# Optimization experiments

Hardware: AMD Instinct MI355X
Metric: run time of the kernel (lower is better)

Reference implementation:

```python
import jax, jax.numpy as jnp
import numpy as np

B, N, D = 4, 4096, 1024       # batch, seq_len, model dim
H, DH = 16, 64                # heads, dim per head
W = 256                       # sliding window size (causal: keys in [i-W+1, i])


def setup_inputs() -> dict:
    key = jax.random.key(0)
    k1, k2, k3 = jax.random.split(key, 3)
    x = jax.random.normal(k1, (B, N, D), dtype=jnp.float32)
    w_qkv = jax.random.normal(k2, (D, 3 * H * DH), dtype=jnp.float32) * (D ** -0.5)
    w_out = jax.random.normal(k3, (H * DH, D), dtype=jnp.float32) * ((H * DH) ** -0.5)
    return {"x": x, "w_qkv": w_qkv, "w_out": w_out}


def _sliding_window_attn(q, k, v):
    """Causal sliding-window attention, banded (block-local) computation.

    q,k,v: [BH, N, DH]; query i attends keys j with i-W+1 <= j <= i.
    Identical math to masking a full NxN score matrix with -finfo.max then softmax.
    """
    BH, n, dh = q.shape
    nb = n // W  # N is a multiple of W
    qb = q.reshape(BH, nb, W, dh)
    pad = jnp.zeros((BH, W, dh), q.dtype)
    kp = jnp.concatenate([pad, k], axis=1).reshape(BH, nb + 1, W, dh)
    vp = jnp.concatenate([pad, v], axis=1).reshape(BH, nb + 1, W, dh)
    # each query block sees previous block + current block of keys -> 2W keys
    kw = jnp.concatenate([kp[:, :-1], kp[:, 1:]], axis=2)  # [BH, nb, 2W, dh]
    vw = jnp.concatenate([vp[:, :-1], vp[:, 1:]], axis=2)
    scores = jnp.einsum('bnqd,bnkd->bnqk', qb, kw)  # [BH, nb, W, 2W]
    blk = jnp.arange(nb)[:, None, None]
    ii = jnp.arange(W)[None, :, None]
    jj = jnp.arange(2 * W)[None, None, :]
    # absolute key index = blk*W + jj - W ; absolute query index = blk*W + ii
    mask = (jj - W <= ii) & (jj >= ii + 1) & (blk * W + jj - W >= 0)
    neg = -jnp.finfo(scores.dtype).max  # matches torch max_neg_value
    scores = jnp.where(mask[None], scores, neg)
    attn = jax.nn.softmax(scores, axis=-1)
    out = jnp.einsum('bnqk,bnkd->bnqd', attn, vw)
    return out.reshape(BH, n, dh)


def reference(x, w_qkv, w_out):
    b, n, d = x.shape
    qkv = x @ w_qkv                      # [b, n, 3*H*DH]
    q, k, v = jnp.split(qkv, 3, axis=-1)

    def to_heads(t):  # b n (h d) -> (b h) n d
        return t.reshape(b, n, H, DH).transpose(0, 2, 1, 3).reshape(b * H, n, DH)

    q, k, v = map(to_heads, (q, k, v))
    q = q * (DH ** -0.5)                 # default scale = dim_head**-0.5
    out = _sliding_window_attn(q, k, v)  # [(b h), n, DH]
    out = out.reshape(b, H, n, DH).transpose(0, 2, 1, 3).reshape(b, n, H * DH)
    return out @ w_out
```

## Files before the change

kernel.cpp:

```cpp
#include <hip/hip_runtime.h>

typedef __attribute__((ext_vector_type(8))) short short8;
typedef __attribute__((ext_vector_type(4))) float floatx4;

#define AS1(p) ((const __attribute__((address_space(1))) void*)(uintptr_t)(p))
#define AS3(p) ((__attribute__((address_space(3))) void*)(unsigned int)(uintptr_t)(p))

__device__ __forceinline__ unsigned short f2bf(float f) {
    union { float f; unsigned int u; } v; v.f = f;
    unsigned int u = v.u;
    unsigned int r = (u + 0x7FFFu + ((u >> 16) & 1u)) >> 16;
    return (unsigned short)r;
}

__device__ __forceinline__ int pk_bf16(float a, float b) {
#if __has_builtin(__builtin_amdgcn_cvt_pk_bf16_f32)
    auto r = __builtin_amdgcn_cvt_pk_bf16_f32(a, b);
    int out; __builtin_memcpy(&out, &r, sizeof(int)); return out;
#else
    return (int)f2bf(a) | ((int)f2bf(b) << 16);
#endif
}

__global__ __launch_bounds__(256) void cvt_x(const float* __restrict__ src,
                                             unsigned short* __restrict__ dst, int n4) {
    int i = blockIdx.x * blockDim.x + threadIdx.x;
    if (i < n4) {
        float4 v = ((const float4*)src)[i];
        int2 o = {pk_bf16(v.x, v.y), pk_bf16(v.z, v.w)};
        ((int2*)dst)[i] = o;
    }
}

__global__ __launch_bounds__(256) void transpose_bf16(const float* __restrict__ src,
                                                      unsigned short* __restrict__ dst,
                                                      int R, int C) {
    __shared__ float tile[32][33];
    int c0 = blockIdx.x * 32, r0 = blockIdx.y * 32;
    int tc = threadIdx.x & 31, tr = (threadIdx.x >> 5) * 4;
#pragma unroll
    for (int i = 0; i < 4; ++i)
        tile[tr + i][tc] = src[(size_t)(r0 + tr + i) * C + c0 + tc];
    __syncthreads();
#pragma unroll
    for (int i = 0; i < 4; ++i)
        dst[(size_t)(c0 + tr + i) * R + r0 + tc] = f2bf(tile[tc][tr + i]);
}

template <bool OUT_BF16>
__global__ __launch_bounds__(512, 2) void gemm_bt256(const unsigned short* __restrict__ A,
                                                     const unsigned short* __restrict__ Bt,
                                                     void* __restrict__ Cout,
                                                     int M, int N, int K, int nbx) {
    __shared__ unsigned short Al[4][256 * 32];
    __shared__ unsigned short Bl[4][256 * 32];

    const int tid = threadIdx.x;
    const int wave = tid >> 6, lane = tid & 63, quad = lane >> 4, l15 = lane & 15;
    const int wm = wave >> 2, wn = wave & 3;

    const int nwg = (int)gridDim.x;
    const int q8 = nwg >> 3;
    const int wgid = (int)blockIdx.x;
    const int swz = (wgid & 7) * q8 + (wgid >> 3);
    const int bm = (swz / nbx) * 256;
    const int bn = (swz % nbx) * 256;

    floatx4 acc[8][4];
    const floatx4 z = {0.f, 0.f, 0.f, 0.f};
#pragma unroll
    for (int mi = 0; mi < 8; ++mi)
#pragma unroll
        for (int ni = 0; ni < 4; ++ni) acc[mi][ni] = z;

    const int d0 = tid, d1 = tid + 512;
    const int r0 = d0 >> 2, c0 = ((d0 & 3) ^ ((d0 >> 3) & 3)) * 8;
    const int r1 = d1 >> 2, c1 = ((d1 & 3) ^ ((d1 >> 3) & 3)) * 8;
    const unsigned short* As0 = A + (size_t)(bm + r0) * K + c0;
    const unsigned short* As1 = A + (size_t)(bm + r1) * K + c1;
    const unsigned short* Bs0 = Bt + (size_t)(bn + r0) * K + c0;
    const unsigned short* Bs1 = Bt + (size_t)(bn + r1) * K + c1;

    auto stageA = [&](int t) {
        const int s = t & 3, ko = t * 32;
        __builtin_amdgcn_global_load_lds(AS1(As0 + ko), AS3(&Al[s][d0 * 8]), 16, 0, 0);
        __builtin_amdgcn_global_load_lds(AS1(As1 + ko), AS3(&Al[s][d1 * 8]), 16, 0, 0);
    };
    auto stageB = [&](int t) {
        const int s = t & 3, ko = t * 32;
        __builtin_amdgcn_global_load_lds(AS1(Bs0 + ko), AS3(&Bl[s][d0 * 8]), 16, 0, 0);
        __builtin_amdgcn_global_load_lds(AS1(Bs1 + ko), AS3(&Bl[s][d1 * 8]), 16, 0, 0);
    };

    const int qc = (quad ^ ((l15 >> 1) & 3)) * 8;
    const int arow = wm * 128 + l15;
    const int brow = wn * 64 + l15;

    stageA(0); stageB(0);
    stageA(1); stageB(1);
    stageA(2); stageB(2);
    asm volatile("s_waitcnt vmcnt(8)" ::: "memory");
    __builtin_amdgcn_s_barrier();

    const int NT = K >> 5;
    for (int t = 0; t < NT; ++t) {
        const int s = t & 3;
        const unsigned short* Alp = Al[s];
        const unsigned short* Blp = Bl[s];
        short8 af[4], bf[4];

#pragma unroll
        for (int mi = 0; mi < 4; ++mi)
            af[mi] = *(const short8*)&Alp[(arow + mi * 16) * 32 + qc];
#pragma unroll
        for (int ni = 0; ni < 4; ++ni)
            bf[ni] = *(const short8*)&Blp[(brow + ni * 16) * 32 + qc];
        if (t + 3 < NT) stageA(t + 3);
        __builtin_amdgcn_s_barrier();
        __builtin_amdgcn_s_setprio(1);
#pragma unroll
        for (int mi = 0; mi < 4; ++mi)
#pragma unroll
            for (int ni = 0; ni < 4; ++ni)
                acc[mi][ni] = __builtin_amdgcn_mfma_f32_16x16x32_bf16(bf[ni], af[mi], acc[mi][ni], 0, 0, 0);
        __builtin_amdgcn_s_setprio(0);
        __builtin_amdgcn_s_barrier();

#pragma unroll
        for (int mi = 0; mi < 4; ++mi)
            af[mi] = *(const short8*)&Alp[(arow + 64 + mi * 16) * 32 + qc];
        if (t + 3 < NT) stageB(t + 3);
        __builtin_amdgcn_s_barrier();
        __builtin_amdgcn_s_setprio(1);
#pragma unroll
        for (int mi = 0; mi < 4; ++mi)
#pragma unroll
            for (int ni = 0; ni < 4; ++ni)
                acc[4 + mi][ni] = __builtin_amdgcn_mfma_f32_16x16x32_bf16(bf[ni], af[mi], acc[4 + mi][ni], 0, 0, 0);
        __builtin_amdgcn_s_setprio(0);

        if (t + 3 < NT)      asm volatile("s_waitcnt vmcnt(8)" ::: "memory");
        else if (t + 2 < NT) asm volatile("s_waitcnt vmcnt(4)" ::: "memory");
        else if (t + 1 < NT) asm volatile("s_waitcnt vmcnt(0)" ::: "memory");
        __builtin_amdgcn_s_barrier();
    }

#pragma unroll
    for (int mi = 0; mi < 8; ++mi) {
        const size_t row = (size_t)(bm + wm * 128 + mi * 16 + l15);
#pragma unroll
        for (int ni = 0; ni < 4; ++ni) {
            const size_t col = (size_t)(bn + wn * 64 + ni * 16 + quad * 4);
            if (OUT_BF16) {
                int2 val = {pk_bf16(acc[mi][ni][0], acc[mi][ni][1]),
                            pk_bf16(acc[mi][ni][2], acc[mi][ni][3])};
                *(int2*)((unsigned short*)Cout + row * N + col) = val;
            } else {
                *(float4*)((float*)Cout + row * N + col) = *(const float4*)&acc[mi][ni];
            }
        }
    }
}

__global__ __launch_bounds__(256, 3) void attn_swin(const unsigned short* __restrict__ qkv,
                                                    unsigned short* __restrict__ attn_out) {
    __shared__ unsigned short Klds[2][64 * 72];
    __shared__ unsigned short Vtl[2][64 * 72];

    const int blk = blockIdx.x, bh = blockIdx.y;
    const int b = bh >> 4, h = bh & 15;
    const int tid = threadIdx.x;
    const int wave = tid >> 6, lane = tid & 63, quad = lane >> 4, l15 = lane & 15;
    const int pair = wave >> 1;
    const int qoff = (wave & 1) * 32;
    const int qi_base = blk * 128 + wave * 32;
    const size_t seqbase = (size_t)b * 4096;

    short8 qf[2][2];
#pragma unroll
    for (int qt = 0; qt < 2; ++qt)
#pragma unroll
        for (int ks = 0; ks < 2; ++ks)
            qf[qt][ks] = *(const short8*)(qkv + (seqbase + qi_base + qt * 16 + l15) * 3072
                                          + h * 64 + ks * 32 + quad * 8);

    floatx4 o[2][4];
    const floatx4 z = {0.f, 0.f, 0.f, 0.f};
    float m_run[2], l_run[2];
#pragma unroll
    for (int qt = 0; qt < 2; ++qt) {
#pragma unroll
        for (int dt = 0; dt < 4; ++dt) o[qt][dt] = z;
        m_run[qt] = -1.0e30f; l_run[qt] = 0.f;
    }

    const int kwin0 = blk * 128 - 256;
    const int c0 = (blk >= 2) ? 0 : (4 - 2 * blk);
    const int cLo = pair, cHi = pair + 4;
    const int sk_key = tid >> 2, sk_g = (tid & 3) * 16;
    const int sv_key = tid & 63, sv_dg = (tid >> 6) * 16;
    const float SC = 0.18033688f;

    const int addrA = (((quad & 1) << 5) + l15) << 2;
    const int addrB = addrA + 64;
    const bool hiq = quad >= 2;

    int4 kvreg[4];
    auto load_kv = [&](int k0) {
        const int4* sk = (const int4*)(qkv + (seqbase + k0 + sk_key) * 3072 + 1024 + h * 64 + sk_g);
        kvreg[0] = sk[0]; kvreg[1] = sk[1];
        const int4* sv = (const int4*)(qkv + (seqbase + k0 + sv_key) * 3072 + 2048 + h * 64 + sv_dg);
        kvreg[2] = sv[0]; kvreg[3] = sv[1];
    };
    auto write_kv = [&](int buf) {
        *(int4*)&Klds[buf][sk_key * 72 + sk_g]     = kvreg[0];
        *(int4*)&Klds[buf][sk_key * 72 + sk_g + 8] = kvreg[1];
        union { unsigned short s[16]; int4 q[2]; } t;
        t.q[0] = kvreg[2]; t.q[1] = kvreg[3];
#pragma unroll
        for (int i = 0; i < 16; ++i) Vtl[buf][(sv_dg + i) * 72 + sv_key] = t.s[i];
    };

    load_kv(kwin0 + c0 * 64);
    write_kv(0);

    for (int c = c0; c < 6; ++c) {
        const int buf = (c - c0) & 1;
        __syncthreads();
        if (c < 5) load_kv(kwin0 + (c + 1) * 64);

        if (c >= cLo && c <= cHi) {
#pragma unroll
            for (int qt = 0; qt < 2; ++qt) {
                floatx4 sT[4];
#pragma unroll
                for (int ni = 0; ni < 4; ++ni) sT[ni] = z;
#pragma unroll
                for (int ks = 0; ks < 2; ++ks) {
#pragma unroll
                    for (int ni = 0; ni < 4; ++ni) {
                        short8 kf = *(const short8*)&Klds[buf][(ni * 16 + l15) * 72 + ks * 32 + quad * 8];
                        sT[ni] = __builtin_amdgcn_mfma_f32_16x16x32_bf16(kf, qf[qt][ks], sT[ni], 0, 0, 0);
                    }
                }

                short8 vf[4][2];
#pragma unroll
                for (int dt = 0; dt < 4; ++dt)
#pragma unroll
                    for (int ks = 0; ks < 2; ++ks)
                        vf[dt][ks] = *(const short8*)&Vtl[buf][(dt * 16 + l15) * 72 + ks * 32 + quad * 8];

                const int i64 = qoff + qt * 16 + l15;
                if (c == cLo) {
#pragma unroll
                    for (int ni = 0; ni < 4; ++ni) {
                        int jb = ni * 16 + quad * 4;
#pragma unroll
                        for (int r = 0; r < 4; ++r)
                            if (jb + r < i64 + 1) sT[ni][r] = -3.0e38f;
                    }
                } else if (c == cHi) {
#pragma unroll
                    for (int ni = 0; ni < 4; ++ni) {
                        int jb = ni * 16 + quad * 4;
#pragma unroll
                        for (int r = 0; r < 4; ++r)
                            if (jb + r > i64) sT[ni][r] = -3.0e38f;
                    }
                }

                float mx = -3.0e38f;
#pragma unroll
                for (int ni = 0; ni < 4; ++ni)
#pragma unroll
                    for (int r = 0; r < 4; ++r) mx = fmaxf(mx, sT[ni][r]);
                mx = fmaxf(mx, __shfl_xor(mx, 16));
                mx = fmaxf(mx, __shfl_xor(mx, 32));
                float mn = fmaxf(m_run[qt], mx * SC);
                float alpha = __builtin_amdgcn_exp2f(m_run[qt] - mn);
                m_run[qt] = mn;

                float ls = 0.f;
                int Pk[4][2];
#pragma unroll
                for (int ni = 0; ni < 4; ++ni) {
                    float p0 = __builtin_amdgcn_exp2f(fmaf(sT[ni][0], SC, -mn));
                    float p1 = __builtin_amdgcn_exp2f(fmaf(sT[ni][1], SC, -mn));
                    float p2 = __builtin_amdgcn_exp2f(fmaf(sT[ni][2], SC, -mn));
                    float p3 = __builtin_amdgcn_exp2f(fmaf(sT[ni][3], SC, -mn));
                    ls += (p0 + p1) + (p2 + p3);
                    Pk[ni][0] = pk_bf16(p0, p1);
                    Pk[ni][1] = pk_bf16(p2, p3);
                }
                ls += __shfl_xor(ls, 16);
                ls += __shfl_xor(ls, 32);
                l_run[qt] = l_run[qt] * alpha + ls;
#pragma unroll
                for (int dt = 0; dt < 4; ++dt)
#pragma unroll
                    for (int r = 0; r < 4; ++r) o[qt][dt][r] *= alpha;

#pragma unroll
                for (int ks = 0; ks < 2; ++ks) {
                    int a0 = __builtin_amdgcn_ds_bpermute(addrA, Pk[2 * ks][0]);
                    int b0 = __builtin_amdgcn_ds_bpermute(addrA, Pk[2 * ks + 1][0]);
                    int a1 = __builtin_amdgcn_ds_bpermute(addrA, Pk[2 * ks][1]);
                    int b1 = __builtin_amdgcn_ds_bpermute(addrA, Pk[2 * ks + 1][1]);
                    int a2 = __builtin_amdgcn_ds_bpermute(addrB, Pk[2 * ks][0]);
                    int b2 = __builtin_amdgcn_ds_bpermute(addrB, Pk[2 * ks + 1][0]);
                    int a3 = __builtin_amdgcn_ds_bpermute(addrB, Pk[2 * ks][1]);
                    int b3 = __builtin_amdgcn_ds_bpermute(addrB, Pk[2 * ks + 1][1]);
                    union { int i[4]; short8 v; } u;
                    u.i[0] = hiq ? b0 : a0;
                    u.i[1] = hiq ? b1 : a1;
                    u.i[2] = hiq ? b2 : a2;
                    u.i[3] = hiq ? b3 : a3;
#pragma unroll
                    for (int dt = 0; dt < 4; ++dt)
                        o[qt][dt] = __builtin_amdgcn_mfma_f32_16x16x32_bf16(vf[dt][ks], u.v, o[qt][dt], 0, 0, 0);
                }
            }
        }

        if (c < 5) write_kv(buf ^ 1);
    }

#pragma unroll
    for (int qt = 0; qt < 2; ++qt) {
        float rl = __builtin_amdgcn_rcpf(l_run[qt]);
        size_t rowb = (seqbase + qi_base + qt * 16 + l15) * 1024 + h * 64;
#pragma unroll
        for (int dt = 0; dt < 4; ++dt) {
            int2 val = {pk_bf16(o[qt][dt][0] * rl, o[qt][dt][1] * rl),
                        pk_bf16(o[qt][dt][2] * rl, o[qt][dt][3] * rl)};
            *(int2*)(attn_out + rowb + dt * 16 + quad * 4) = val;
        }
    }
}

extern "C" void kernel_launch(void* const* d_in, const int* in_sizes, int n_in,
                              void* d_out, int out_size, void* d_ws, size_t ws_size,
                              hipStream_t stream) {
    const float* x     = (const float*)d_in[0];
    const float* w_qkv = (const float*)d_in[1];
    const float* w_out = (const float*)d_in[2];
    float* out = (float*)d_out;

    unsigned short* xb    = (unsigned short*)d_ws;
    unsigned short* wqkvT = xb    + (size_t)16384 * 1024;
    unsigned short* woutT = wqkvT + (size_t)3072 * 1024;
    unsigned short* qkv   = woutT + (size_t)1024 * 1024;
    unsigned short* attn  = qkv   + (size_t)16384 * 3072;

    cvt_x<<<16384, 256, 0, stream>>>(x, xb, 4194304);
    transpose_bf16<<<dim3(96, 32), 256, 0, stream>>>(w_qkv, wqkvT, 1024, 3072);
    transpose_bf16<<<dim3(32, 32), 256, 0, stream>>>(w_out, woutT, 1024, 1024);
    gemm_bt256<true><<<768, 512, 0, stream>>>(xb, wqkvT, qkv, 16384, 3072, 1024, 12);
    attn_swin<<<dim3(32, 64), 256, 0, stream>>>(qkv, attn);
    gemm_bt256<false><<<256, 512, 0, stream>>>(attn, woutT, out, 16384, 1024, 1024, 4);
}
```

Measured before the change: 363.1 us.

## Software-pipeline LDS fragment loads across K iterations in bf16 GEMM

Restructures the GEMM main loop so LDS fragments for the next K-tile are loaded into double-buffered registers while the current tile's MFMAs run, cutting one barrier per iteration. The loop is manually unrolled by two to alternate register buffers, and the vmcnt waits are retuned to the new issue order. The cost is higher register pressure from the two fragment sets, and the unroll by two assumes NT is even.

```diff
diff --git a/kernel.cpp b/kernel.cpp
--- a/kernel.cpp
+++ b/kernel.cpp
@@ -81,6 +81,8 @@
     const unsigned short* Bs0 = Bt + (size_t)(bn + r0) * K + c0;
     const unsigned short* Bs1 = Bt + (size_t)(bn + r1) * K + c1;
 
+    const int NT = K >> 5;
+
     auto stageA = [&](int t) {
         const int s = t & 3, ko = t * 32;
         __builtin_amdgcn_global_load_lds(AS1(As0 + ko), AS3(&Al[s][d0 * 8]), 16, 0, 0);
@@ -102,47 +104,58 @@
     asm volatile("s_waitcnt vmcnt(8)" ::: "memory");
     __builtin_amdgcn_s_barrier();
 
-    const int NT = K >> 5;
-    for (int t = 0; t < NT; ++t) {
+    short8 afA[4], bfA[4], afB[4], bfB[4];
+#pragma unroll
+    for (int mi = 0; mi < 4; ++mi)
+        afA[mi] = *(const short8*)&Al[0][(arow + mi * 16) * 32 + qc];
+#pragma unroll
+    for (int ni = 0; ni < 4; ++ni)
+        bfA[ni] = *(const short8*)&Bl[0][(brow + ni * 16) * 32 + qc];
+
+    auto body = [&](int t, short8 (&caf)[4], short8 (&cbf)[4],
+                    short8 (&naf)[4], short8 (&nbf)[4]) {
         const int s = t & 3;
         const unsigned short* Alp = Al[s];
-        const unsigned short* Blp = Bl[s];
-        short8 af[4], bf[4];
-
+        if (t + 3 < NT) stageA(t + 3);
+        short8 af1[4];
 #pragma unroll
         for (int mi = 0; mi < 4; ++mi)
-            af[mi] = *(const short8*)&Alp[(arow + mi * 16) * 32 + qc];
-#pragma unroll
-        for (int ni = 0; ni < 4; ++ni)
-            bf[ni] = *(const short8*)&Blp[(brow + ni * 16) * 32 + qc];
-        if (t + 3 < NT) stageA(t + 3);
+            af1[mi] = *(const short8*)&Alp[(arow + 64 + mi * 16) * 32 + qc];
+        __builtin_amdgcn_s_setprio(1);
+#pragma unroll
+        for (int mi = 0; mi < 4; ++mi)
+#pragma unroll
+            for (int ni = 0; ni < 4; ++ni)
+                acc[mi][ni] = __builtin_amdgcn_mfma_f32_16x16x32_bf16(cbf[ni], caf[mi], acc[mi][ni], 0, 0, 0);
+        __builtin_amdgcn_s_setprio(0);
+        if (t + 3 < NT)       asm volatile("s_waitcnt vmcnt(6)" ::: "memory");
+        else if (t + 3 == NT) asm volatile("s_waitcnt vmcnt(4)" ::: "memory");
+        else                  asm volatile("s_waitcnt vmcnt(0)" ::: "memory");
         __builtin_amdgcn_s_barrier();
+        if (t + 1 < NT) {
+            const unsigned short* Aln = Al[(t + 1) & 3];
+            const unsigned short* Bln = Bl[(t + 1) & 3];
+#pragma unroll
+            for (int mi = 0; mi < 4; ++mi)
+                naf[mi] = *(const short8*)&Aln[(arow + mi * 16) * 32 + qc];
+#pragma unroll
+            for (int ni = 0; ni < 4; ++ni)
+                nbf[ni] = *(const short8*)&Bln[(brow + ni * 16) * 32 + qc];
+        }
+        if (t + 3 < NT) stageB(t + 3);
         __builtin_amdgcn_s_setprio(1);
 #pragma unroll
         for (int mi = 0; mi < 4; ++mi)
 #pragma unroll
             for (int ni = 0; ni < 4; ++ni)
-                acc[mi][ni] = __builtin_amdgcn_mfma_f32_16x16x32_bf16(bf[ni], af[mi], acc[mi][ni], 0, 0, 0);
+                acc[4 + mi][ni] = __builtin_amdgcn_mfma_f32_16x16x32_bf16(cbf[ni], af1[mi], acc[4 + mi][ni], 0, 0, 0);
         __builtin_amdgcn_s_setprio(0);
         __builtin_amdgcn_s_barrier();
-
-#pragma unroll
-        for (int mi = 0; mi < 4; ++mi)
-            af[mi] = *(const short8*)&Alp[(arow + 64 + mi * 16) * 32 + qc];
-        if (t + 3 < NT) stageB(t + 3);
-        __builtin_amdgcn_s_barrier();
-        __builtin_amdgcn_s_setprio(1);
-#pragma unroll
-        for (int mi = 0; mi < 4; ++mi)
-#pragma unroll
-            for (int ni = 0; ni < 4; ++ni)
-                acc[4 + mi][ni] = __builtin_amdgcn_mfma_f32_16x16x32_bf16(bf[ni], af[mi], acc[4 + mi][ni], 0, 0, 0);
-        __builtin_amdgcn_s_setprio(0);
-
-        if (t + 3 < NT)      asm volatile("s_waitcnt vmcnt(8)" ::: "memory");
-        else if (t + 2 < NT) asm volatile("s_waitcnt vmcnt(4)" ::: "memory");
-        else if (t + 1 < NT) asm volatile("s_waitcnt vmcnt(0)" ::: "memory");
-        __builtin_amdgcn_s_barrier();
+    };
+
+    for (int tt = 0; tt < NT; tt += 2) {
+        body(tt,     afA, bfA, afB, bfB);
+        body(tt + 1, afB, bfB, afA, bfA);
     }
 
 #pragma unroll
```

After: 362.4 us. No clear change (-0.2%).

## Restructure GEMM mainloop to K=64 tiles with half-tile double-buffered staging

Applied to the files above, without the earlier changes.

The GEMM mainloop now stages 64-wide K tiles into a 2-stage LDS buffer, split into 128-row halves, instead of 32-wide tiles in a 4-stage ring. Each K step runs four MFMA phases, and the A and B halves are prefetched at different distances (A one tile ahead, B two tiles ahead). The LDS swizzle is widened to an 8-way XOR to match. The aim is fewer loop iterations and barriers per unit of K work, with loads interleaved between MFMA phases. The cost is more register fragments live at once and tighter vmcnt and barrier ordering, where any mistake could cause races.

```diff
diff --git a/kernel.cpp b/kernel.cpp
--- a/kernel.cpp
+++ b/kernel.cpp
@@ -52,8 +52,8 @@
                                                      const unsigned short* __restrict__ Bt,
                                                      void* __restrict__ Cout,
                                                      int M, int N, int K, int nbx) {
-    __shared__ unsigned short Al[4][256 * 32];
-    __shared__ unsigned short Bl[4][256 * 32];
+    __shared__ unsigned short Ah[2][2][128 * 64];
+    __shared__ unsigned short Bh[2][2][128 * 64];
 
     const int tid = threadIdx.x;
     const int wave = tid >> 6, lane = tid & 63, quad = lane >> 4, l15 = lane & 15;
@@ -73,76 +73,110 @@
 #pragma unroll
         for (int ni = 0; ni < 4; ++ni) acc[mi][ni] = z;
 
-    const int d0 = tid, d1 = tid + 512;
-    const int r0 = d0 >> 2, c0 = ((d0 & 3) ^ ((d0 >> 3) & 3)) * 8;
-    const int r1 = d1 >> 2, c1 = ((d1 & 3) ^ ((d1 >> 3) & 3)) * 8;
-    const unsigned short* As0 = A + (size_t)(bm + r0) * K + c0;
-    const unsigned short* As1 = A + (size_t)(bm + r1) * K + c1;
-    const unsigned short* Bs0 = Bt + (size_t)(bn + r0) * K + c0;
-    const unsigned short* Bs1 = Bt + (size_t)(bn + r1) * K + c1;
-
-    auto stageA = [&](int t) {
-        const int s = t & 3, ko = t * 32;
-        __builtin_amdgcn_global_load_lds(AS1(As0 + ko), AS3(&Al[s][d0 * 8]), 16, 0, 0);
-        __builtin_amdgcn_global_load_lds(AS1(As1 + ko), AS3(&Al[s][d1 * 8]), 16, 0, 0);
+    const int r0 = tid >> 3;
+    const int cc = ((tid & 7) ^ ((tid >> 3) & 7)) * 8;
+    const unsigned short* Asrc = A + (size_t)(bm + r0) * K + cc;
+    const unsigned short* Bsrc = Bt + (size_t)(bn + r0) * K + cc;
+
+    const int NT = K >> 6;
+
+    auto stageA = [&](int t, int h) {
+        const unsigned short* s0 = Asrc + (size_t)h * 128 * K + t * 64;
+        unsigned short* d = &Ah[t & 1][h][tid * 8];
+        __builtin_amdgcn_global_load_lds(AS1(s0), AS3(d), 16, 0, 0);
+        __builtin_amdgcn_global_load_lds(AS1(s0 + (size_t)64 * K), AS3(d + 512 * 8), 16, 0, 0);
     };
-    auto stageB = [&](int t) {
-        const int s = t & 3, ko = t * 32;
-        __builtin_amdgcn_global_load_lds(AS1(Bs0 + ko), AS3(&Bl[s][d0 * 8]), 16, 0, 0);
-        __builtin_amdgcn_global_load_lds(AS1(Bs1 + ko), AS3(&Bl[s][d1 * 8]), 16, 0, 0);
+    auto stageB = [&](int t, int h) {
+        const unsigned short* s0 = Bsrc + (size_t)h * 128 * K + t * 64;
+        unsigned short* d = &Bh[t & 1][h][tid * 8];
+        __builtin_amdgcn_global_load_lds(AS1(s0), AS3(d), 16, 0, 0);
+        __builtin_amdgcn_global_load_lds(AS1(s0 + (size_t)64 * K), AS3(d + 512 * 8), 16, 0, 0);
     };
 
-    const int qc = (quad ^ ((l15 >> 1) & 3)) * 8;
-    const int arow = wm * 128 + l15;
-    const int brow = wn * 64 + l15;
-
-    stageA(0); stageB(0);
-    stageA(1); stageB(1);
-    stageA(2); stageB(2);
-    asm volatile("s_waitcnt vmcnt(8)" ::: "memory");
+    const int kc0 = ((quad     ) ^ (l15 & 7)) * 8;
+    const int kc1 = ((quad ^ 4) ^ (l15 & 7)) * 8;
+    const int brb = (wn & 1) * 64;
+
+    stageA(0, 0); stageA(0, 1);
+    stageB(0, 0); stageB(0, 1);
+    if (NT > 1) {
+        stageB(1, 0); stageB(1, 1);
+        asm volatile("s_waitcnt vmcnt(4)" ::: "memory");
+    } else {
+        asm volatile("s_waitcnt vmcnt(0)" ::: "memory");
+    }
     __builtin_amdgcn_s_barrier();
 
-    const int NT = K >> 5;
     for (int t = 0; t < NT; ++t) {
-        const int s = t & 3;
-        const unsigned short* Alp = Al[s];
-        const unsigned short* Blp = Bl[s];
-        short8 af[4], bf[4];
-
-#pragma unroll
-        for (int mi = 0; mi < 4; ++mi)
-            af[mi] = *(const short8*)&Alp[(arow + mi * 16) * 32 + qc];
+        const int s = t & 1;
+        const unsigned short* Ap = &Ah[s][wm][0];
+        const unsigned short* Bp = &Bh[s][wn >> 1][0];
+        short8 a0[4], a1[4], b0[4], b1[4];
+
+#pragma unroll
+        for (int mi = 0; mi < 4; ++mi)
+            a0[mi] = *(const short8*)&Ap[(mi * 16 + l15) * 64 + kc0];
 #pragma unroll
         for (int ni = 0; ni < 4; ++ni)
-            bf[ni] = *(const short8*)&Blp[(brow + ni * 16) * 32 + qc];
-        if (t + 3 < NT) stageA(t + 3);
+            b0[ni] = *(const short8*)&Bp[(brb + ni * 16 + l15) * 64 + kc0];
+        if (t + 1 < NT) stageA(t + 1, 0);
         __builtin_amdgcn_s_barrier();
         __builtin_amdgcn_s_setprio(1);
 #pragma unroll
         for (int mi = 0; mi < 4; ++mi)
 #pragma unroll
             for (int ni = 0; ni < 4; ++ni)
-                acc[mi][ni] = __builtin_amdgcn_mfma_f32_16x16x32_bf16(bf[ni], af[mi], acc[mi][ni], 0, 0, 0);
+                acc[mi][ni] = __builtin_amdgcn_mfma_f32_16x16x32_bf16(b0[ni], a0[mi], acc[mi][ni], 0, 0, 0);
         __builtin_amdgcn_s_setprio(0);
         __builtin_amdgcn_s_barrier();
 
 #pragma unroll
-        for (int mi = 0; mi < 4; ++mi)
-            af[mi] = *(const short8*)&Alp[(arow + 64 + mi * 16) * 32 + qc];
-        if (t + 3 < NT) stageB(t + 3);
+        for (int ni = 0; ni < 4; ++ni)
+            b1[ni] = *(const short8*)&Bp[(brb + ni * 16 + l15) * 64 + kc1];
+#pragma unroll
+        for (int mi = 0; mi < 4; ++mi)
+            a1[mi] = *(const short8*)&Ap[(64 + mi * 16 + l15) * 64 + kc0];
+        if (t + 1 < NT) stageA(t + 1, 1);
         __builtin_amdgcn_s_barrier();
         __builtin_amdgcn_s_setprio(1);
 #pragma unroll
         for (int mi = 0; mi < 4; ++mi)
 #pragma unroll
             for (int ni = 0; ni < 4; ++ni)
-                acc[4 + mi][ni] = __builtin_amdgcn_mfma_f32_16x16x32_bf16(bf[ni], af[mi], acc[4 + mi][ni], 0, 0, 0);
+                acc[4 + mi][ni] = __builtin_amdgcn_mfma_f32_16x16x32_bf16(b0[ni], a1[mi], acc[4 + mi][ni], 0, 0, 0);
         __builtin_amdgcn_s_setprio(0);
-
-        if (t + 3 < NT)      asm volatile("s_waitcnt vmcnt(8)" ::: "memory");
-        else if (t + 2 < NT) asm volatile("s_waitcnt vmcnt(4)" ::: "memory");
+        __builtin_amdgcn_s_barrier();
+
+#pragma unroll
+        for (int mi = 0; mi < 4; ++mi)
+            a0[mi] = *(const short8*)&Ap[(mi * 16 + l15) * 64 + kc1];
+        if (t + 2 < NT) stageB(t + 2, 0);
+        __builtin_amdgcn_s_barrier();
+        __builtin_amdgcn_s_setprio(1);
+#pragma unroll
+        for (int mi = 0; mi < 4; ++mi)
+#pragma unroll
+            for (int ni = 0; ni < 4; ++ni)
+                acc[mi][ni] = __builtin_amdgcn_mfma_f32_16x16x32_bf16(b1[ni], a0[mi], acc[mi][ni], 0, 0, 0);
+        __builtin_amdgcn_s_setprio(0);
+        __builtin_amdgcn_s_barrier();
+
+#pragma unroll
+        for (int mi = 0; mi < 4; ++mi)
+            a1[mi] = *(const short8*)&Ap[(64 + mi * 16 + l15) * 64 + kc1];
+        if (t + 2 < NT) stageB(t + 2, 1);
+        __builtin_amdgcn_s_barrier();
+        __builtin_amdgcn_s_setprio(1);
+#pragma unroll
+        for (int mi = 0; mi < 4; ++mi)
+#pragma unroll
+            for (int ni = 0; ni < 4; ++ni)
+                acc[4 + mi][ni] = __builtin_amdgcn_mfma_f32_16x16x32_bf16(b1[ni], a1[mi], acc[4 + mi][ni], 0, 0, 0);
+        __builtin_amdgcn_s_setprio(0);
+
+        if (t + 2 < NT)      asm volatile("s_waitcnt vmcnt(4)" ::: "memory");
         else if (t + 1 < NT) asm volatile("s_waitcnt vmcnt(0)" ::: "memory");
-        __builtin_amdgcn_s_barrier();
+        if (t + 1 < NT) __builtin_amdgcn_s_barrier();
     }
 
 #pragma unroll
```

Measured after the change: 361.0 us. Within noise of the previous version (-0.6%).

## Shrink GEMM tile to 128x256 with 4 waves and double-buffered LDS

Applied to the files above, without the earlier changes.

Replaces the 256x256, 8-wave, 4-stage GEMM with a 128x256 tile computed by 4 waves, each owning a 128x64 slice. LDS staging drops from four stages to two, with a single combined stage per k-step and a full vmcnt(0) wait before the barrier. The grids double so more workgroups can spread across CUs. In exchange, each tile reuses loaded data less, and the shallower prefetch can expose global-load latency.

```diff
diff --git a/kernel.cpp b/kernel.cpp
--- a/kernel.cpp
+++ b/kernel.cpp
@@ -48,22 +48,21 @@
 }
 
 template <bool OUT_BF16>
-__global__ __launch_bounds__(512, 2) void gemm_bt256(const unsigned short* __restrict__ A,
+__global__ __launch_bounds__(256, 2) void gemm_bt128(const unsigned short* __restrict__ A,
                                                      const unsigned short* __restrict__ Bt,
                                                      void* __restrict__ Cout,
                                                      int M, int N, int K, int nbx) {
-    __shared__ unsigned short Al[4][256 * 32];
-    __shared__ unsigned short Bl[4][256 * 32];
+    __shared__ unsigned short Asm[2][128 * 32];
+    __shared__ unsigned short Bsm[2][256 * 32];
 
     const int tid = threadIdx.x;
-    const int wave = tid >> 6, lane = tid & 63, quad = lane >> 4, l15 = lane & 15;
-    const int wm = wave >> 2, wn = wave & 3;
+    const int wn = tid >> 6, lane = tid & 63, quad = lane >> 4, l15 = lane & 15;
 
     const int nwg = (int)gridDim.x;
     const int q8 = nwg >> 3;
     const int wgid = (int)blockIdx.x;
     const int swz = (wgid & 7) * q8 + (wgid >> 3);
-    const int bm = (swz / nbx) * 256;
+    const int bm = (swz / nbx) * 128;
     const int bn = (swz % nbx) * 256;
 
     floatx4 acc[8][4];
@@ -73,81 +72,75 @@
 #pragma unroll
         for (int ni = 0; ni < 4; ++ni) acc[mi][ni] = z;
 
-    const int d0 = tid, d1 = tid + 512;
-    const int r0 = d0 >> 2, c0 = ((d0 & 3) ^ ((d0 >> 3) & 3)) * 8;
-    const int r1 = d1 >> 2, c1 = ((d1 & 3) ^ ((d1 >> 3) & 3)) * 8;
-    const unsigned short* As0 = A + (size_t)(bm + r0) * K + c0;
-    const unsigned short* As1 = A + (size_t)(bm + r1) * K + c1;
-    const unsigned short* Bs0 = Bt + (size_t)(bn + r0) * K + c0;
-    const unsigned short* Bs1 = Bt + (size_t)(bn + r1) * K + c1;
-
-    auto stageA = [&](int t) {
-        const int s = t & 3, ko = t * 32;
-        __builtin_amdgcn_global_load_lds(AS1(As0 + ko), AS3(&Al[s][d0 * 8]), 16, 0, 0);
-        __builtin_amdgcn_global_load_lds(AS1(As1 + ko), AS3(&Al[s][d1 * 8]), 16, 0, 0);
+    const int dA0 = tid, dA1 = tid + 256;
+    const int rA0 = dA0 >> 2, cA0 = ((dA0 & 3) ^ ((dA0 >> 3) & 3)) * 8;
+    const int rA1 = dA1 >> 2, cA1 = ((dA1 & 3) ^ ((dA1 >> 3) & 3)) * 8;
+    const unsigned short* Asrc0 = A + (size_t)(bm + rA0) * K + cA0;
+    const unsigned short* Asrc1 = A + (size_t)(bm + rA1) * K + cA1;
+    const unsigned short* Bsrc[4];
+    int dB[4];
+#pragma unroll
+    for (int j = 0; j < 4; ++j) {
+        dB[j] = tid + j * 256;
+        const int r = dB[j] >> 2, c = ((dB[j] & 3) ^ ((dB[j] >> 3) & 3)) * 8;
+        Bsrc[j] = Bt + (size_t)(bn + r) * K + c;
+    }
+
+    const int NT = K >> 5;
+
+    auto stage = [&](int t) {
+        const int s = t & 1, ko = t * 32;
+        __builtin_amdgcn_global_load_lds(AS1(Asrc0 + ko), AS3(&Asm[s][dA0 * 8]), 16, 0, 0);
+        __builtin_amdgcn_global_load_lds(AS1(Asrc1 + ko), AS3(&Asm[s][dA1 * 8]), 16, 0, 0);
+#pragma unroll
+        for (int j = 0; j < 4; ++j)
+            __builtin_amdgcn_global_load_lds(AS1(Bsrc[j] + ko), AS3(&Bsm[s][dB[j] * 8]), 16, 0, 0);
     };
-    auto stageB = [&](int t) {
-        const int s = t & 3, ko = t * 32;
-        __builtin_amdgcn_global_load_lds(AS1(Bs0 + ko), AS3(&Bl[s][d0 * 8]), 16, 0, 0);
-        __builtin_amdgcn_global_load_lds(AS1(Bs1 + ko), AS3(&Bl[s][d1 * 8]), 16, 0, 0);
-    };
 
     const int qc = (quad ^ ((l15 >> 1) & 3)) * 8;
-    const int arow = wm * 128 + l15;
     const int brow = wn * 64 + l15;
 
-    stageA(0); stageB(0);
-    stageA(1); stageB(1);
-    stageA(2); stageB(2);
-    asm volatile("s_waitcnt vmcnt(8)" ::: "memory");
+    stage(0);
+    asm volatile("s_waitcnt vmcnt(0)" ::: "memory");
     __builtin_amdgcn_s_barrier();
 
-    const int NT = K >> 5;
     for (int t = 0; t < NT; ++t) {
-        const int s = t & 3;
-        const unsigned short* Alp = Al[s];
-        const unsigned short* Blp = Bl[s];
-        short8 af[4], bf[4];
-
+        const int s = t & 1;
+        const unsigned short* Ap = Asm[s];
+        const unsigned short* Bp = Bsm[s];
+        if (t + 1 < NT) stage(t + 1);
+
+        short8 b[4], a0[4], a1[4];
+#pragma unroll
+        for (int ni = 0; ni < 4; ++ni)
+            b[ni] = *(const short8*)&Bp[(brow + ni * 16) * 32 + qc];
 #pragma unroll
         for (int mi = 0; mi < 4; ++mi)
-            af[mi] = *(const short8*)&Alp[(arow + mi * 16) * 32 + qc];
-#pragma unroll
-        for (int ni = 0; ni < 4; ++ni)
-            bf[ni] = *(const short8*)&Blp[(brow + ni * 16) * 32 + qc];
-        if (t + 3 < NT) stageA(t + 3);
+            a0[mi] = *(const short8*)&Ap[(mi * 16 + l15) * 32 + qc];
+#pragma unroll
+        for (int mi = 0; mi < 4; ++mi)
+            a1[mi] = *(const short8*)&Ap[(64 + mi * 16 + l15) * 32 + qc];
+
+        __builtin_amdgcn_s_setprio(1);
+#pragma unroll
+        for (int mi = 0; mi < 4; ++mi)
+#pragma unroll
+            for (int ni = 0; ni < 4; ++ni)
+                acc[mi][ni] = __builtin_amdgcn_mfma_f32_16x16x32_bf16(b[ni], a0[mi], acc[mi][ni], 0, 0, 0);
+#pragma unroll
+        for (int mi = 0; mi < 4; ++mi)
+#pragma unroll
+            for (int ni = 0; ni < 4; ++ni)
+                acc[4 + mi][ni] = __builtin_amdgcn_mfma_f32_16x16x32_bf16(b[ni], a1[mi], acc[4 + mi][ni], 0, 0, 0);
+        __builtin_amdgcn_s_setprio(0);
+
+        asm volatile("s_waitcnt vmcnt(0)" ::: "memory");
         __builtin_amdgcn_s_barrier();
-        __builtin_amdgcn_s_setprio(1);
-#pragma unroll
-        for (int mi = 0; mi < 4; ++mi)
-#pragma unroll
-            for (int ni = 0; ni < 4; ++ni)
-                acc[mi][ni] = __builtin_amdgcn_mfma_f32_16x16x32_bf16(bf[ni], af[mi], acc[mi][ni], 0, 0, 0);
-        __builtin_amdgcn_s_setprio(0);
-        __builtin_amdgcn_s_barrier();
-
-#pragma unroll
-        for (int mi = 0; mi < 4; ++mi)
-            af[mi] = *(const short8*)&Alp[(arow + 64 + mi * 16) * 32 + qc];
-        if (t + 3 < NT) stageB(t + 3);
-        __builtin_amdgcn_s_barrier();
-        __builtin_amdgcn_s_setprio(1);
-#pragma unroll
-        for (int mi = 0; mi < 4; ++mi)
-#pragma unroll
-            for (int ni = 0; ni < 4; ++ni)
-                acc[4 + mi][ni] = __builtin_amdgcn_mfma_f32_16x16x32_bf16(bf[ni], af[mi], acc[4 + mi][ni], 0, 0, 0);
-        __builtin_amdgcn_s_setprio(0);
-
-        if (t + 3 < NT)      asm volatile("s_waitcnt vmcnt(8)" ::: "memory");
-        else if (t + 2 < NT) asm volatile("s_waitcnt vmcnt(4)" ::: "memory");
-        else if (t + 1 < NT) asm volatile("s_waitcnt vmcnt(0)" ::: "memory");
-        __builtin_amdgcn_s_barrier();
     }
 
 #pragma unroll
     for (int mi = 0; mi < 8; ++mi) {
-        const size_t row = (size_t)(bm + wm * 128 + mi * 16 + l15);
+        const size_t row = (size_t)(bm + mi * 16 + l15);
 #pragma unroll
         for (int ni = 0; ni < 4; ++ni) {
             const size_t col = (size_t)(bn + wn * 64 + ni * 16 + quad * 4);
@@ -356,7 +349,7 @@
     cvt_x<<<16384, 256, 0, stream>>>(x, xb, 4194304);
     transpose_bf16<<<dim3(96, 32), 256, 0, stream>>>(w_qkv, wqkvT, 1024, 3072);
     transpose_bf16<<<dim3(32, 32), 256, 0, stream>>>(w_out, woutT, 1024, 1024);
-    gemm_bt256<true><<<768, 512, 0, stream>>>(xb, wqkvT, qkv, 16384, 3072, 1024, 12);
+    gemm_bt128<true><<<1536, 256, 0, stream>>>(xb, wqkvT, qkv, 16384, 3072, 1024, 12);
     attn_swin<<<dim3(32, 64), 256, 0, stream>>>(qkv, attn);
-    gemm_bt256<false><<<256, 512, 0, stream>>>(attn, woutT, out, 16384, 1024, 1024, 4);
-}
+    gemm_bt128<false><<<512, 256, 0, stream>>>(attn, woutT, out, 16384, 1024, 1024, 4);
+}
```

Result: faster. 354.9 us (-2.2%).
